# Performance work log

Measured on AMD Instinct MI355X. Metric: run time of the kernel, lower is better.

## Reference

```python
import jax, jax.numpy as jnp
import numpy as np

N_NODES = 1_000_000
N_EDGES = 16_000_000
BATCH = 1_000_000
EMBED_DIM = 3


def setup_inputs() -> dict:
    key = jax.random.key(0)
    ks = jax.random.split(key, 11)
    edge_index = jax.random.randint(ks[0], (2, N_EDGES), 0, N_NODES, dtype=jnp.int32)
    edge_weight = jax.random.uniform(ks[1], (N_EDGES,), dtype=jnp.float32) + 0.1
    home = jax.random.randint(ks[2], (BATCH,), 0, N_NODES, dtype=jnp.int32)
    away = jax.random.randint(ks[3], (BATCH,), 0, N_NODES, dtype=jnp.int32)
    emb = jax.random.normal(ks[4], (N_NODES, EMBED_DIM), dtype=jnp.float32)
    w_conv = jax.random.normal(ks[5], (3, 3), dtype=jnp.float32) * 0.5
    b_conv = jax.random.normal(ks[6], (3,), dtype=jnp.float32) * 0.1
    w1 = jax.random.normal(ks[7], (6, 6), dtype=jnp.float32) * 0.4
    b1 = jax.random.normal(ks[8], (6,), dtype=jnp.float32) * 0.1
    w3 = jax.random.normal(ks[9], (6, 3), dtype=jnp.float32) * 0.4
    b3 = jax.random.normal(ks[10], (3,), dtype=jnp.float32) * 0.1
    return {"edge_index": edge_index, "edge_weight": edge_weight, "home": home,
            "away": away, "emb": emb, "w_conv": w_conv, "b_conv": b_conv,
            "w1": w1, "b1": b1, "w3": w3, "b3": b3}


def reference(edge_index, edge_weight, home, away, emb, w_conv, b_conv, w1, b1, w3, b3):
    n = emb.shape[0]
    row, col = edge_index[0], edge_index[1]
    # gcn_norm (symmetric, add_self_loops=False): deg over target nodes
    deg = jax.ops.segment_sum(edge_weight, col, num_segments=n)
    dinv = jnp.where(deg > 0, jax.lax.rsqrt(jnp.where(deg > 0, deg, 1.0)), 0.0)
    norm = dinv[row] * edge_weight * dinv[col]  # [E]
    x = emb @ w_conv                            # [N,3] transformed features
    msg = norm[:, None] * x[row]                # [E,3] gather + scale
    agg = jax.ops.segment_sum(msg, col, num_segments=n) + b_conv  # [N,3]
    x = jax.nn.leaky_relu(agg)                  # conv1 output
    h = jnp.concatenate([x[home], x[away]], axis=-1)  # [B,6]
    h = jax.nn.leaky_relu(h @ w1 + b1)          # lin1
    h = jax.nn.leaky_relu(h @ w3 + b3)          # lin3 -> [B,3]
    return jax.nn.log_softmax(h, axis=0)        # LogSoftmax over dim=0 as in source
```

## Files before the change

### kernel.cpp

```cpp
#include <hip/hip_runtime.h>
#include <math.h>

#define NN 1000000
#define NE 16000000
#define NB 1000000
#define NEQ (NE / 4)
#define BN 4096
#define NBUCK 245
#define NBUCKR 256
#define NBLK 1024
#define SSPLIT 4
#define CMASK 0xFFFFFu

#define FPS 512.0f
#define FPINV (1.0f / 512.0f)
#define FBIAS (1 << 20)
#define FMASK 0x1FFFFFu
#define ACC_INIT 0x4000020000100000ULL

typedef int   i32x4 __attribute__((ext_vector_type(4)));
typedef float f32x4 __attribute__((ext_vector_type(4)));

__device__ __forceinline__ float leaky(float v) { return v > 0.f ? v : 0.01f * v; }

#define ATOMF(p, v) unsafeAtomicAdd((p), (v))

__device__ __forceinline__ unsigned int pack_bf32(float x, float y, float z) {
    float m = fmaxf(fmaxf(fabsf(x), fabsf(y)), fabsf(z));
    int ex = ((int)(__float_as_uint(m) >> 23) & 0xFF) - 126;
    ex = min(max(ex, -20), 11);
    float scale = __uint_as_float((unsigned int)(135 - ex) << 23);
    int qx = min(max(__float2int_rn(x * scale), -255), 255);
    int qy = min(max(__float2int_rn(y * scale), -255), 255);
    int qz = min(max(__float2int_rn(z * scale), -255), 255);
    return ((unsigned int)(qx & 0x1FF)) | ((unsigned int)(qy & 0x1FF) << 9) |
           ((unsigned int)(qz & 0x1FF) << 18) | ((unsigned int)(ex + 20) << 27);
}

__device__ __forceinline__ float3 unpack_bf32(unsigned int u) {
    int qx = ((int)(u << 23)) >> 23;
    int qy = ((int)(u << 14)) >> 23;
    int qz = ((int)(u << 5)) >> 23;
    int ex = (int)(u >> 27) - 20;
    float s = __uint_as_float((unsigned int)(ex + 119) << 23);
    return make_float3(qx * s, qy * s, qz * s);
}

__device__ __forceinline__ void atomicMaxF(float* addr, float val) {
    unsigned int* ia = (unsigned int*)addr;
    unsigned int old = *ia;
    while (true) {
        float f = __uint_as_float(old);
        if (f >= val) break;
        unsigned int prev = atomicCAS(ia, old, __float_as_uint(val));
        if (prev == old) break;
        old = prev;
    }
}

__global__ void init_stats(float* stats) {
    int t = threadIdx.x;
    if (t < 3) stats[t] = -1e30f;
    else if (t < 6) stats[t] = 0.f;
}

__global__ __launch_bounds__(256) void count_kernel(const i32x4* __restrict__ col4,
                                                    unsigned int* __restrict__ HG) {
    __shared__ unsigned int h[4][NBUCKR];
    int wave = threadIdx.x >> 6;
    for (int t = threadIdx.x; t < 4 * NBUCKR; t += 256) ((unsigned int*)h)[t] = 0u;
    __syncthreads();
    int stride = gridDim.x * 256;
    for (int i = blockIdx.x * 256 + threadIdx.x; i < NEQ; i += stride) {
        i32x4 c = __builtin_nontemporal_load(col4 + i);
        atomicAdd(&h[wave][((unsigned int)c.x) >> 12], 1u);
        atomicAdd(&h[wave][((unsigned int)c.y) >> 12], 1u);
        atomicAdd(&h[wave][((unsigned int)c.z) >> 12], 1u);
        atomicAdd(&h[wave][((unsigned int)c.w) >> 12], 1u);
    }
    __syncthreads();
    HG[(size_t)threadIdx.x * NBLK + blockIdx.x] =
        h[0][threadIdx.x] + h[1][threadIdx.x] + h[2][threadIdx.x] + h[3][threadIdx.x];
}

__global__ __launch_bounds__(256) void scan_sum(const unsigned int* __restrict__ HG,
                                                unsigned int* __restrict__ part) {
    const unsigned int* p = HG + (size_t)blockIdx.x * NBLK;
    unsigned int s = 0;
    for (int i = threadIdx.x; i < NBLK; i += 256) s += p[i];
    #pragma unroll
    for (int off = 32; off > 0; off >>= 1) s += __shfl_down(s, off);
    __shared__ unsigned int sm[4];
    int wave = threadIdx.x >> 6, lane = threadIdx.x & 63;
    if (lane == 0) sm[wave] = s;
    __syncthreads();
    if (threadIdx.x == 0) part[blockIdx.x] = sm[0] + sm[1] + sm[2] + sm[3];
}

__global__ void scan_part(unsigned int* part) {
    __shared__ unsigned int tmp[256];
    int t = threadIdx.x;
    unsigned int v = part[t];
    tmp[t] = v;
    __syncthreads();
    for (int off = 1; off < 256; off <<= 1) {
        unsigned int add = (t >= off) ? tmp[t - off] : 0u;
        __syncthreads();
        tmp[t] += add;
        __syncthreads();
    }
    part[t] = tmp[t] - v;
}

__global__ __launch_bounds__(256) void scan_apply(unsigned int* __restrict__ HG,
                                                  const unsigned int* __restrict__ part) {
    __shared__ unsigned int vals[NBLK];
    __shared__ unsigned int ts[256];
    int t = threadIdx.x;
    unsigned int* p = HG + (size_t)blockIdx.x * NBLK;
    for (int i = t; i < NBLK; i += 256) vals[i] = p[i];
    __syncthreads();
    unsigned int a0 = vals[4 * t], a1 = vals[4 * t + 1], a2 = vals[4 * t + 2], a3 = vals[4 * t + 3];
    unsigned int ls = a0 + a1 + a2 + a3;
    ts[t] = ls;
    __syncthreads();
    for (int off = 1; off < 256; off <<= 1) {
        unsigned int add = (t >= off) ? ts[t - off] : 0u;
        __syncthreads();
        ts[t] += add;
        __syncthreads();
    }
    unsigned int base = part[blockIdx.x] + ts[t] - ls;
    p[4 * t] = base;
    p[4 * t + 1] = base + a0;
    p[4 * t + 2] = base + a0 + a1;
    p[4 * t + 3] = base + a0 + a1 + a2;
}

__global__ __launch_bounds__(256) void scatter_kernel(const i32x4* __restrict__ row4,
                                                      const i32x4* __restrict__ col4,
                                                      const f32x4* __restrict__ w4,
                                                      const unsigned int* __restrict__ HG,
                                                      uint2* __restrict__ rec) {
    __shared__ unsigned int pos[NBUCKR];
    pos[threadIdx.x] = HG[(size_t)threadIdx.x * NBLK + blockIdx.x];
    __syncthreads();
    int stride = gridDim.x * 256;
    for (int i = blockIdx.x * 256 + threadIdx.x; i < NEQ; i += stride) {
        i32x4 r = __builtin_nontemporal_load(row4 + i);
        i32x4 c = __builtin_nontemporal_load(col4 + i);
        f32x4 w = __builtin_nontemporal_load(w4 + i);
        {
            unsigned int cu = (unsigned int)c.x;
            unsigned int p = atomicAdd(&pos[cu >> 12], 1u);
            rec[p] = make_uint2((unsigned int)r.x | ((cu & 4095u) << 20), __float_as_uint(w.x));
        }
        {
            unsigned int cu = (unsigned int)c.y;
            unsigned int p = atomicAdd(&pos[cu >> 12], 1u);
            rec[p] = make_uint2((unsigned int)r.y | ((cu & 4095u) << 20), __float_as_uint(w.y));
        }
        {
            unsigned int cu = (unsigned int)c.z;
            unsigned int p = atomicAdd(&pos[cu >> 12], 1u);
            rec[p] = make_uint2((unsigned int)r.z | ((cu & 4095u) << 20), __float_as_uint(w.z));
        }
        {
            unsigned int cu = (unsigned int)c.w;
            unsigned int p = atomicAdd(&pos[cu >> 12], 1u);
            rec[p] = make_uint2((unsigned int)r.w | ((cu & 4095u) << 20), __float_as_uint(w.w));
        }
    }
}

__global__ __launch_bounds__(512) void bucket_deg_kernel(const unsigned long long* __restrict__ rec,
                                                         const unsigned int* __restrict__ HG,
                                                         float* __restrict__ deg_g) {
    __shared__ float degl[BN];
    int b = blockIdx.x % NBUCK;
    int sp = blockIdx.x / NBUCK;
    for (int t = threadIdx.x; t < BN; t += 512) degl[t] = 0.f;
    unsigned int s0 = HG[(size_t)b * NBLK];
    unsigned int e0 = HG[(size_t)(b + 1) * NBLK];
    unsigned int n = e0 - s0;
    unsigned int beg = s0 + (unsigned int)((unsigned long long)n * sp / SSPLIT);
    unsigned int end = s0 + (unsigned int)((unsigned long long)n * (sp + 1) / SSPLIT);
    __syncthreads();
    unsigned int i = beg + threadIdx.x;
    for (; i + 3584 < end; i += 4096) {
        unsigned long long r[8];
        #pragma unroll
        for (int k = 0; k < 8; k++) r[k] = __builtin_nontemporal_load(rec + i + k * 512);
        #pragma unroll
        for (int k = 0; k < 8; k++)
            ATOMF(&degl[((unsigned int)r[k]) >> 20], __uint_as_float((unsigned int)(r[k] >> 32)));
    }
    for (; i < end; i += 512) {
        unsigned long long r0 = __builtin_nontemporal_load(rec + i);
        ATOMF(&degl[((unsigned int)r0) >> 20], __uint_as_float((unsigned int)(r0 >> 32)));
    }
    __syncthreads();
    int node0 = b * BN;
    for (int t = threadIdx.x; t < BN; t += 512) {
        float v = degl[t];
        if (v != 0.f) ATOMF(&deg_g[node0 + t], v);
    }
}

__global__ __launch_bounds__(256) void node1_kernel(const float* __restrict__ deg_g,
                                                    const float* __restrict__ emb,
                                                    const float* __restrict__ w_conv,
                                                    float* __restrict__ dinv,
                                                    unsigned int* __restrict__ y) {
    int g = blockIdx.x * 256 + threadIdx.x;
    if (g >= NN) return;
    float d = deg_g[g];
    float di = d > 0.f ? rsqrtf(d) : 0.f;
    dinv[g] = di;
    float e0 = emb[3 * g], e1 = emb[3 * g + 1], e2 = emb[3 * g + 2];
    float x0 = e0 * w_conv[0] + e1 * w_conv[3] + e2 * w_conv[6];
    float x1 = e0 * w_conv[1] + e1 * w_conv[4] + e2 * w_conv[7];
    float x2 = e0 * w_conv[2] + e1 * w_conv[5] + e2 * w_conv[8];
    y[g] = pack_bf32(di * x0, di * x1, di * x2);
}

__global__ __launch_bounds__(512) void bucket_agg_kernel(const unsigned long long* __restrict__ rec,
                                                         const unsigned int* __restrict__ HG,
                                                         const unsigned int* __restrict__ y,
                                                         float* __restrict__ acc_g) {
    __shared__ unsigned long long accp[BN];
    int b = blockIdx.x % NBUCK;
    int sp = blockIdx.x / NBUCK;
    for (int t = threadIdx.x; t < BN; t += 512) accp[t] = ACC_INIT;
    unsigned int s0 = HG[(size_t)b * NBLK];
    unsigned int e0 = HG[(size_t)(b + 1) * NBLK];
    unsigned int n = e0 - s0;
    unsigned int beg = s0 + (unsigned int)((unsigned long long)n * sp / SSPLIT);
    unsigned int end = s0 + (unsigned int)((unsigned long long)n * (sp + 1) / SSPLIT);
    __syncthreads();
    unsigned int i = beg + threadIdx.x;
    for (; i + 3584 < end; i += 4096) {
        unsigned long long r[8];
        #pragma unroll
        for (int k = 0; k < 8; k++) r[k] = __builtin_nontemporal_load(rec + i + k * 512);
        unsigned int yu[8];
        #pragma unroll
        for (int k = 0; k < 8; k++) yu[k] = y[((unsigned int)r[k]) & CMASK];
        #pragma unroll
        for (int k = 0; k < 8; k++) {
            float ws = __uint_as_float((unsigned int)(r[k] >> 32)) * FPS;
            float3 yv = unpack_bf32(yu[k]);
            long long q0 = (long long)__float2int_rn(ws * yv.x);
            long long q1 = (long long)__float2int_rn(ws * yv.y);
            long long q2 = (long long)__float2int_rn(ws * yv.z);
            unsigned long long term = (unsigned long long)((q2 << 42) + (q1 << 21) + q0);
            unsigned int c = ((unsigned int)r[k]) >> 20;
            atomicAdd(&accp[c], term);
        }
    }
    for (; i < end; i += 512) {
        unsigned long long r0 = __builtin_nontemporal_load(rec + i);
        float ws = __uint_as_float((unsigned int)(r0 >> 32)) * FPS;
        float3 yv = unpack_bf32(y[((unsigned int)r0) & CMASK]);
        long long q0 = (long long)__float2int_rn(ws * yv.x);
        long long q1 = (long long)__float2int_rn(ws * yv.y);
        long long q2 = (long long)__float2int_rn(ws * yv.z);
        unsigned long long term = (unsigned long long)((q2 << 42) + (q1 << 21) + q0);
        unsigned int c = ((unsigned int)r0) >> 20;
        atomicAdd(&accp[c], term);
    }
    __syncthreads();
    size_t base = (size_t)b * BN * 3;
    for (int t = threadIdx.x; t < BN; t += 512) {
        unsigned long long v = accp[t];
        if (v != ACC_INIT) {
            int f0 = (int)((unsigned int)(v & FMASK)) - FBIAS;
            int f1 = (int)((unsigned int)((v >> 21) & FMASK)) - FBIAS;
            int f2 = (int)((unsigned int)((v >> 42) & FMASK)) - FBIAS;
            if (f0) ATOMF(&acc_g[base + 3 * t + 0], (float)f0 * FPINV);
            if (f1) ATOMF(&acc_g[base + 3 * t + 1], (float)f1 * FPINV);
            if (f2) ATOMF(&acc_g[base + 3 * t + 2], (float)f2 * FPINV);
        }
    }
}

__global__ __launch_bounds__(256) void node2_kernel(const float* __restrict__ acc_g,
                                                    const float* __restrict__ dinv,
                                                    const float* __restrict__ b_conv,
                                                    unsigned int* __restrict__ xf) {
    int g = blockIdx.x * 256 + threadIdx.x;
    if (g >= NN) return;
    float di = dinv[g];
    float a0 = acc_g[3 * (size_t)g], a1 = acc_g[3 * (size_t)g + 1], a2 = acc_g[3 * (size_t)g + 2];
    xf[g] = pack_bf32(leaky(di * a0 + b_conv[0]),
                      leaky(di * a1 + b_conv[1]),
                      leaky(di * a2 + b_conv[2]));
}

__global__ __launch_bounds__(256) void batch_kernel(const i32x4* __restrict__ home4,
                                                    const i32x4* __restrict__ away4,
                                                    const unsigned int* __restrict__ xf,
                                                    const float* __restrict__ w1,
                                                    const float* __restrict__ b1,
                                                    const float* __restrict__ w3,
                                                    const float* __restrict__ b3,
                                                    float4* __restrict__ out4,
                                                    float* __restrict__ stats, int nq) {
    int i = blockIdx.x * blockDim.x + threadIdx.x;
    float m0 = -1e30f, m1 = -1e30f, m2 = -1e30f;
    if (i < nq) {
        float W1[36], B1[6], W3[18], B3[3];
        #pragma unroll
        for (int k = 0; k < 36; k++) W1[k] = w1[k];
        #pragma unroll
        for (int k = 0; k < 6; k++) B1[k] = b1[k];
        #pragma unroll
        for (int k = 0; k < 18; k++) W3[k] = w3[k];
        #pragma unroll
        for (int k = 0; k < 3; k++) B3[k] = b3[k];

        i32x4 hh = __builtin_nontemporal_load(home4 + i);
        i32x4 aa = __builtin_nontemporal_load(away4 + i);
        int hs[4] = {hh.x, hh.y, hh.z, hh.w};
        int as_[4] = {aa.x, aa.y, aa.z, aa.w};
        float o[12];
        #pragma unroll
        for (int e = 0; e < 4; e++) {
            float3 xh = unpack_bf32(xf[hs[e]]);
            float3 xa = unpack_bf32(xf[as_[e]]);
            float h[6] = {xh.x, xh.y, xh.z, xa.x, xa.y, xa.z};
            float l1v[6];
            #pragma unroll
            for (int j = 0; j < 6; j++) {
                float s = B1[j];
                #pragma unroll
                for (int k = 0; k < 6; k++) s += h[k] * W1[k * 6 + j];
                l1v[j] = leaky(s);
            }
            float o3[3];
            #pragma unroll
            for (int j = 0; j < 3; j++) {
                float s = B3[j];
                #pragma unroll
                for (int k = 0; k < 6; k++) s += l1v[k] * W3[k * 3 + j];
                o3[j] = leaky(s);
            }
            o[3 * e + 0] = o3[0];
            o[3 * e + 1] = o3[1];
            o[3 * e + 2] = o3[2];
            m0 = fmaxf(m0, o3[0]);
            m1 = fmaxf(m1, o3[1]);
            m2 = fmaxf(m2, o3[2]);
        }
        #pragma unroll
        for (int q = 0; q < 3; q++)
            out4[3 * (size_t)i + q] = make_float4(o[4 * q], o[4 * q + 1], o[4 * q + 2], o[4 * q + 3]);
    }
    #pragma unroll
    for (int off = 32; off > 0; off >>= 1) {
        m0 = fmaxf(m0, __shfl_down(m0, off));
        m1 = fmaxf(m1, __shfl_down(m1, off));
        m2 = fmaxf(m2, __shfl_down(m2, off));
    }
    __shared__ float sm[3][4];
    int wave = threadIdx.x >> 6, lane = threadIdx.x & 63;
    if (lane == 0) { sm[0][wave] = m0; sm[1][wave] = m1; sm[2][wave] = m2; }
    __syncthreads();
    if (threadIdx.x == 0) {
        atomicMaxF(&stats[0], fmaxf(fmaxf(sm[0][0], sm[0][1]), fmaxf(sm[0][2], sm[0][3])));
        atomicMaxF(&stats[1], fmaxf(fmaxf(sm[1][0], sm[1][1]), fmaxf(sm[1][2], sm[1][3])));
        atomicMaxF(&stats[2], fmaxf(fmaxf(sm[2][0], sm[2][1]), fmaxf(sm[2][2], sm[2][3])));
    }
}

__global__ __launch_bounds__(256) void sumexp_kernel(const float4* __restrict__ out4,
                                                     float* __restrict__ stats, int nq) {
    float mx0 = stats[0], mx1 = stats[1], mx2 = stats[2];
    int i = blockIdx.x * blockDim.x + threadIdx.x;
    float s0 = 0.f, s1 = 0.f, s2 = 0.f;
    if (i < nq) {
        float4 v = out4[i];
        float vals[4] = {v.x, v.y, v.z, v.w};
        int c = (4 * i) % 3;
        #pragma unroll
        for (int e = 0; e < 4; e++) {
            float mv = (c == 0) ? mx0 : ((c == 1) ? mx1 : mx2);
            float ee = expf(vals[e] - mv);
            if (c == 0) s0 += ee; else if (c == 1) s1 += ee; else s2 += ee;
            c = (c == 2) ? 0 : (c + 1);
        }
    }
    #pragma unroll
    for (int off = 32; off > 0; off >>= 1) {
        s0 += __shfl_down(s0, off);
        s1 += __shfl_down(s1, off);
        s2 += __shfl_down(s2, off);
    }
    __shared__ float sm[3][4];
    int wave = threadIdx.x >> 6, lane = threadIdx.x & 63;
    if (lane == 0) { sm[0][wave] = s0; sm[1][wave] = s1; sm[2][wave] = s2; }
    __syncthreads();
    if (threadIdx.x == 0) {
        ATOMF(&stats[3], sm[0][0] + sm[0][1] + sm[0][2] + sm[0][3]);
        ATOMF(&stats[4], sm[1][0] + sm[1][1] + sm[1][2] + sm[1][3]);
        ATOMF(&stats[5], sm[2][0] + sm[2][1] + sm[2][2] + sm[2][3]);
    }
}

__global__ __launch_bounds__(256) void final_kernel(float4* __restrict__ out4,
                                                    const float* __restrict__ stats, int nq) {
    float o0 = stats[0] + logf(stats[3]);
    float o1 = stats[1] + logf(stats[4]);
    float o2 = stats[2] + logf(stats[5]);
    int i = blockIdx.x * blockDim.x + threadIdx.x;
    if (i >= nq) return;
    float4 v = out4[i];
    float vals[4] = {v.x, v.y, v.z, v.w};
    int c = (4 * i) % 3;
    #pragma unroll
    for (int e = 0; e < 4; e++) {
        vals[e] -= (c == 0) ? o0 : ((c == 1) ? o1 : o2);
        c = (c == 2) ? 0 : (c + 1);
    }
    out4[i] = make_float4(vals[0], vals[1], vals[2], vals[3]);
}

extern "C" void kernel_launch(void* const* d_in, const int* in_sizes, int n_in,
                              void* d_out, int out_size, void* d_ws, size_t ws_size,
                              hipStream_t stream) {
    const int*   edge_index  = (const int*)d_in[0];
    const float* edge_weight = (const float*)d_in[1];
    const int*   home        = (const int*)d_in[2];
    const int*   away        = (const int*)d_in[3];
    const float* emb         = (const float*)d_in[4];
    const float* w_conv      = (const float*)d_in[5];
    const float* b_conv      = (const float*)d_in[6];
    const float* w1          = (const float*)d_in[7];
    const float* b1          = (const float*)d_in[8];
    const float* w3          = (const float*)d_in[9];
    const float* b3          = (const float*)d_in[10];
    float* out = (float*)d_out;

    char* ws = (char*)d_ws;
    uint2*        rec   = (uint2*)(ws);
    unsigned int* HG    = (unsigned int*)(ws + 128000000);
    unsigned int* part  = (unsigned int*)(ws + 129048576);
    float*        deg_g = (float*)(ws + 129049600);
    float*        dinv  = (float*)(ws + 133063680);
    unsigned int* y     = (unsigned int*)(ws + 137063680);
    float*        acc_g = (float*)(ws + 141063680);
    unsigned int* xf    = (unsigned int*)(ws + 153105920);
    float*        stats = (float*)(ws + 157105920);

    const int* row = edge_index;
    const int* col = edge_index + NE;

    init_stats<<<1, 64, 0, stream>>>(stats);
    hipMemsetAsync(deg_g, 0, 4014080, stream);
    hipMemsetAsync(acc_g, 0, 12042240, stream);

    count_kernel<<<NBLK, 256, 0, stream>>>((const i32x4*)col, HG);
    scan_sum<<<NBUCKR, 256, 0, stream>>>(HG, part);
    scan_part<<<1, 256, 0, stream>>>(part);
    scan_apply<<<NBUCKR, 256, 0, stream>>>(HG, part);
    scatter_kernel<<<NBLK, 256, 0, stream>>>((const i32x4*)row, (const i32x4*)col,
                                             (const f32x4*)edge_weight, HG, rec);

    bucket_deg_kernel<<<NBUCK * SSPLIT, 512, 0, stream>>>((const unsigned long long*)rec, HG, deg_g);
    node1_kernel<<<(NN + 255) / 256, 256, 0, stream>>>(deg_g, emb, w_conv, dinv, y);
    bucket_agg_kernel<<<NBUCK * SSPLIT, 512, 0, stream>>>((const unsigned long long*)rec, HG, y, acc_g);
    node2_kernel<<<(NN + 255) / 256, 256, 0, stream>>>(acc_g, dinv, b_conv, xf);

    const int BQ = NB / 4;
    const int OQ = (NB * 3) / 4;
    batch_kernel<<<(BQ + 255) / 256, 256, 0, stream>>>((const i32x4*)home, (const i32x4*)away, xf,
                                                       w1, b1, w3, b3, (float4*)out, stats, BQ);
    sumexp_kernel<<<(OQ + 255) / 256, 256, 0, stream>>>((const float4*)out, stats, OQ);
    final_kernel<<<(OQ + 255) / 256, 256, 0, stream>>>((float4*)out, stats, OQ);
}
```

Before: 814.5 us.

## Use 1024-node buckets owned by one block, writing results directly without global atomics

Buckets shrink from 4096 to 1024 nodes, and each bucket is now handled by exactly one block instead of being split four ways. Because of that, the degree and aggregate results are stored straight to global memory, which removes the two memsets and the global float atomics. The packed 21-bit fixed-point accumulator is decoded with signed arithmetic in node2 instead of a biased init value. In exchange there are four times as many histogram buckets, so the HG scan and the per-block position tables grow, and load balance across blocks may be worse with no split.

```diff
diff --git a/kernel.cpp b/kernel.cpp
--- a/kernel.cpp
+++ b/kernel.cpp
@@ -5,18 +5,14 @@
 #define NE 16000000
 #define NB 1000000
 #define NEQ (NE / 4)
-#define BN 4096
-#define NBUCK 245
-#define NBUCKR 256
+#define BN 1024
+#define NBUCKA 977
+#define NBUCKR 1024
 #define NBLK 1024
-#define SSPLIT 4
-#define CMASK 0xFFFFFu
+#define RMASK 0xFFFFFu
 
 #define FPS 512.0f
 #define FPINV (1.0f / 512.0f)
-#define FBIAS (1 << 20)
-#define FMASK 0x1FFFFFu
-#define ACC_INIT 0x4000020000100000ULL
 
 typedef int   i32x4 __attribute__((ext_vector_type(4)));
 typedef float f32x4 __attribute__((ext_vector_type(4)));
@@ -73,14 +69,14 @@
     int stride = gridDim.x * 256;
     for (int i = blockIdx.x * 256 + threadIdx.x; i < NEQ; i += stride) {
         i32x4 c = __builtin_nontemporal_load(col4 + i);
-        atomicAdd(&h[wave][((unsigned int)c.x) >> 12], 1u);
-        atomicAdd(&h[wave][((unsigned int)c.y) >> 12], 1u);
-        atomicAdd(&h[wave][((unsigned int)c.z) >> 12], 1u);
-        atomicAdd(&h[wave][((unsigned int)c.w) >> 12], 1u);
-    }
-    __syncthreads();
-    HG[(size_t)threadIdx.x * NBLK + blockIdx.x] =
-        h[0][threadIdx.x] + h[1][threadIdx.x] + h[2][threadIdx.x] + h[3][threadIdx.x];
+        atomicAdd(&h[wave][((unsigned int)c.x) >> 10], 1u);
+        atomicAdd(&h[wave][((unsigned int)c.y) >> 10], 1u);
+        atomicAdd(&h[wave][((unsigned int)c.z) >> 10], 1u);
+        atomicAdd(&h[wave][((unsigned int)c.w) >> 10], 1u);
+    }
+    __syncthreads();
+    for (int b = threadIdx.x; b < NBUCKR; b += 256)
+        HG[(size_t)b * NBLK + blockIdx.x] = h[0][b] + h[1][b] + h[2][b] + h[3][b];
 }
 
 __global__ __launch_bounds__(256) void scan_sum(const unsigned int* __restrict__ HG,
@@ -100,8 +96,9 @@
 __global__ void scan_part(unsigned int* part) {
     __shared__ unsigned int tmp[256];
     int t = threadIdx.x;
-    unsigned int v = part[t];
-    tmp[t] = v;
+    unsigned int v0 = part[4 * t], v1 = part[4 * t + 1], v2 = part[4 * t + 2], v3 = part[4 * t + 3];
+    unsigned int ls = v0 + v1 + v2 + v3;
+    tmp[t] = ls;
     __syncthreads();
     for (int off = 1; off < 256; off <<= 1) {
         unsigned int add = (t >= off) ? tmp[t - off] : 0u;
@@ -109,7 +106,11 @@
         tmp[t] += add;
         __syncthreads();
     }
-    part[t] = tmp[t] - v;
+    unsigned int base = tmp[t] - ls;
+    part[4 * t] = base;
+    part[4 * t + 1] = base + v0;
+    part[4 * t + 2] = base + v0 + v1;
+    part[4 * t + 3] = base + v0 + v1 + v2;
 }
 
 __global__ __launch_bounds__(256) void scan_apply(unsigned int* __restrict__ HG,
@@ -141,34 +142,26 @@
                                                       const i32x4* __restrict__ col4,
                                                       const f32x4* __restrict__ w4,
                                                       const unsigned int* __restrict__ HG,
-                                                      uint2* __restrict__ rec) {
+                                                      unsigned long long* __restrict__ rec) {
     __shared__ unsigned int pos[NBUCKR];
-    pos[threadIdx.x] = HG[(size_t)threadIdx.x * NBLK + blockIdx.x];
+    for (int b = threadIdx.x; b < NBUCKR; b += 256)
+        pos[b] = HG[(size_t)b * NBLK + blockIdx.x];
     __syncthreads();
     int stride = gridDim.x * 256;
     for (int i = blockIdx.x * 256 + threadIdx.x; i < NEQ; i += stride) {
         i32x4 r = __builtin_nontemporal_load(row4 + i);
         i32x4 c = __builtin_nontemporal_load(col4 + i);
         f32x4 w = __builtin_nontemporal_load(w4 + i);
-        {
-            unsigned int cu = (unsigned int)c.x;
-            unsigned int p = atomicAdd(&pos[cu >> 12], 1u);
-            rec[p] = make_uint2((unsigned int)r.x | ((cu & 4095u) << 20), __float_as_uint(w.x));
-        }
-        {
-            unsigned int cu = (unsigned int)c.y;
-            unsigned int p = atomicAdd(&pos[cu >> 12], 1u);
-            rec[p] = make_uint2((unsigned int)r.y | ((cu & 4095u) << 20), __float_as_uint(w.y));
-        }
-        {
-            unsigned int cu = (unsigned int)c.z;
-            unsigned int p = atomicAdd(&pos[cu >> 12], 1u);
-            rec[p] = make_uint2((unsigned int)r.z | ((cu & 4095u) << 20), __float_as_uint(w.z));
-        }
-        {
-            unsigned int cu = (unsigned int)c.w;
-            unsigned int p = atomicAdd(&pos[cu >> 12], 1u);
-            rec[p] = make_uint2((unsigned int)r.w | ((cu & 4095u) << 20), __float_as_uint(w.w));
+        int rr[4] = {r.x, r.y, r.z, r.w};
+        int cc[4] = {c.x, c.y, c.z, c.w};
+        float wf[4] = {w.x, w.y, w.z, w.w};
+        #pragma unroll
+        for (int k = 0; k < 4; k++) {
+            unsigned int cu = (unsigned int)cc[k];
+            unsigned int p = atomicAdd(&pos[cu >> 10], 1u);
+            unsigned long long rk = ((unsigned long long)__float_as_uint(wf[k]) << 32) |
+                                    ((cu & 1023u) << 20) | (unsigned int)rr[k];
+            rec[p] = rk;
         }
     }
 }
@@ -177,14 +170,10 @@
                                                          const unsigned int* __restrict__ HG,
                                                          float* __restrict__ deg_g) {
     __shared__ float degl[BN];
-    int b = blockIdx.x % NBUCK;
-    int sp = blockIdx.x / NBUCK;
+    int b = blockIdx.x;
     for (int t = threadIdx.x; t < BN; t += 512) degl[t] = 0.f;
-    unsigned int s0 = HG[(size_t)b * NBLK];
-    unsigned int e0 = HG[(size_t)(b + 1) * NBLK];
-    unsigned int n = e0 - s0;
-    unsigned int beg = s0 + (unsigned int)((unsigned long long)n * sp / SSPLIT);
-    unsigned int end = s0 + (unsigned int)((unsigned long long)n * (sp + 1) / SSPLIT);
+    unsigned int beg = HG[(size_t)b * NBLK];
+    unsigned int end = HG[(size_t)(b + 1) * NBLK];
     __syncthreads();
     unsigned int i = beg + threadIdx.x;
     for (; i + 3584 < end; i += 4096) {
@@ -193,17 +182,17 @@
         for (int k = 0; k < 8; k++) r[k] = __builtin_nontemporal_load(rec + i + k * 512);
         #pragma unroll
         for (int k = 0; k < 8; k++)
-            ATOMF(&degl[((unsigned int)r[k]) >> 20], __uint_as_float((unsigned int)(r[k] >> 32)));
+            ATOMF(&degl[(((unsigned int)r[k]) >> 20) & 1023u], __uint_as_float((unsigned int)(r[k] >> 32)));
     }
     for (; i < end; i += 512) {
         unsigned long long r0 = __builtin_nontemporal_load(rec + i);
-        ATOMF(&degl[((unsigned int)r0) >> 20], __uint_as_float((unsigned int)(r0 >> 32)));
+        ATOMF(&degl[(((unsigned int)r0) >> 20) & 1023u], __uint_as_float((unsigned int)(r0 >> 32)));
     }
     __syncthreads();
     int node0 = b * BN;
     for (int t = threadIdx.x; t < BN; t += 512) {
-        float v = degl[t];
-        if (v != 0.f) ATOMF(&deg_g[node0 + t], v);
+        int g = node0 + t;
+        if (g < NN) deg_g[g] = degl[t];
     }
 }
 
@@ -227,16 +216,12 @@
 __global__ __launch_bounds__(512) void bucket_agg_kernel(const unsigned long long* __restrict__ rec,
                                                          const unsigned int* __restrict__ HG,
                                                          const unsigned int* __restrict__ y,
-                                                         float* __restrict__ acc_g) {
+                                                         unsigned long long* __restrict__ accq) {
     __shared__ unsigned long long accp[BN];
-    int b = blockIdx.x % NBUCK;
-    int sp = blockIdx.x / NBUCK;
-    for (int t = threadIdx.x; t < BN; t += 512) accp[t] = ACC_INIT;
-    unsigned int s0 = HG[(size_t)b * NBLK];
-    unsigned int e0 = HG[(size_t)(b + 1) * NBLK];
-    unsigned int n = e0 - s0;
-    unsigned int beg = s0 + (unsigned int)((unsigned long long)n * sp / SSPLIT);
-    unsigned int end = s0 + (unsigned int)((unsigned long long)n * (sp + 1) / SSPLIT);
+    int b = blockIdx.x;
+    for (int t = threadIdx.x; t < BN; t += 512) accp[t] = 0ull;
+    unsigned int beg = HG[(size_t)b * NBLK];
+    unsigned int end = HG[(size_t)(b + 1) * NBLK];
     __syncthreads();
     unsigned int i = beg + threadIdx.x;
     for (; i + 3584 < end; i += 4096) {
@@ -245,7 +230,7 @@
         for (int k = 0; k < 8; k++) r[k] = __builtin_nontemporal_load(rec + i + k * 512);
         unsigned int yu[8];
         #pragma unroll
-        for (int k = 0; k < 8; k++) yu[k] = y[((unsigned int)r[k]) & CMASK];
+        for (int k = 0; k < 8; k++) yu[k] = y[((unsigned int)r[k]) & RMASK];
         #pragma unroll
         for (int k = 0; k < 8; k++) {
             float ws = __uint_as_float((unsigned int)(r[k] >> 32)) * FPS;
@@ -254,44 +239,44 @@
             long long q1 = (long long)__float2int_rn(ws * yv.y);
             long long q2 = (long long)__float2int_rn(ws * yv.z);
             unsigned long long term = (unsigned long long)((q2 << 42) + (q1 << 21) + q0);
-            unsigned int c = ((unsigned int)r[k]) >> 20;
+            unsigned int c = (((unsigned int)r[k]) >> 20) & 1023u;
             atomicAdd(&accp[c], term);
         }
     }
     for (; i < end; i += 512) {
         unsigned long long r0 = __builtin_nontemporal_load(rec + i);
         float ws = __uint_as_float((unsigned int)(r0 >> 32)) * FPS;
-        float3 yv = unpack_bf32(y[((unsigned int)r0) & CMASK]);
+        float3 yv = unpack_bf32(y[((unsigned int)r0) & RMASK]);
         long long q0 = (long long)__float2int_rn(ws * yv.x);
         long long q1 = (long long)__float2int_rn(ws * yv.y);
         long long q2 = (long long)__float2int_rn(ws * yv.z);
         unsigned long long term = (unsigned long long)((q2 << 42) + (q1 << 21) + q0);
-        unsigned int c = ((unsigned int)r0) >> 20;
+        unsigned int c = (((unsigned int)r0) >> 20) & 1023u;
         atomicAdd(&accp[c], term);
     }
     __syncthreads();
-    size_t base = (size_t)b * BN * 3;
+    int node0 = b * BN;
     for (int t = threadIdx.x; t < BN; t += 512) {
-        unsigned long long v = accp[t];
-        if (v != ACC_INIT) {
-            int f0 = (int)((unsigned int)(v & FMASK)) - FBIAS;
-            int f1 = (int)((unsigned int)((v >> 21) & FMASK)) - FBIAS;
-            int f2 = (int)((unsigned int)((v >> 42) & FMASK)) - FBIAS;
-            if (f0) ATOMF(&acc_g[base + 3 * t + 0], (float)f0 * FPINV);
-            if (f1) ATOMF(&acc_g[base + 3 * t + 1], (float)f1 * FPINV);
-            if (f2) ATOMF(&acc_g[base + 3 * t + 2], (float)f2 * FPINV);
-        }
-    }
-}
-
-__global__ __launch_bounds__(256) void node2_kernel(const float* __restrict__ acc_g,
+        int g = node0 + t;
+        if (g < NN) accq[g] = accp[t];
+    }
+}
+
+__global__ __launch_bounds__(256) void node2_kernel(const unsigned long long* __restrict__ accq,
                                                     const float* __restrict__ dinv,
                                                     const float* __restrict__ b_conv,
                                                     unsigned int* __restrict__ xf) {
     int g = blockIdx.x * 256 + threadIdx.x;
     if (g >= NN) return;
     float di = dinv[g];
-    float a0 = acc_g[3 * (size_t)g], a1 = acc_g[3 * (size_t)g + 1], a2 = acc_g[3 * (size_t)g + 2];
+    long long T = (long long)accq[g];
+    long long c0 = (T << 43) >> 43;
+    long long T1 = (T - c0) >> 21;
+    long long c1 = (T1 << 43) >> 43;
+    long long c2 = (T1 - c1) >> 21;
+    float a0 = (float)c0 * FPINV;
+    float a1 = (float)c1 * FPINV;
+    float a2 = (float)c2 * FPINV;
     xf[g] = pack_bf32(leaky(di * a0 + b_conv[0]),
                       leaky(di * a1 + b_conv[1]),
                       leaky(di * a2 + b_conv[2]));
@@ -442,22 +427,20 @@
     float* out = (float*)d_out;
 
     char* ws = (char*)d_ws;
-    uint2*        rec   = (uint2*)(ws);
-    unsigned int* HG    = (unsigned int*)(ws + 128000000);
-    unsigned int* part  = (unsigned int*)(ws + 129048576);
-    float*        deg_g = (float*)(ws + 129049600);
-    float*        dinv  = (float*)(ws + 133063680);
-    unsigned int* y     = (unsigned int*)(ws + 137063680);
-    float*        acc_g = (float*)(ws + 141063680);
-    unsigned int* xf    = (unsigned int*)(ws + 153105920);
-    float*        stats = (float*)(ws + 157105920);
+    unsigned long long* rec   = (unsigned long long*)(ws);
+    unsigned int*       HG    = (unsigned int*)(ws + 128000000);
+    unsigned int*       part  = (unsigned int*)(ws + 132194304);
+    float*              deg_g = (float*)(ws + 132198400);
+    float*              dinv  = (float*)(ws + 136198400);
+    unsigned int*       y     = (unsigned int*)(ws + 140198400);
+    unsigned long long* accq  = (unsigned long long*)(ws + 144198400);
+    unsigned int*       xf    = (unsigned int*)(ws + 152198400);
+    float*              stats = (float*)(ws + 156198400);
 
     const int* row = edge_index;
     const int* col = edge_index + NE;
 
     init_stats<<<1, 64, 0, stream>>>(stats);
-    hipMemsetAsync(deg_g, 0, 4014080, stream);
-    hipMemsetAsync(acc_g, 0, 12042240, stream);
 
     count_kernel<<<NBLK, 256, 0, stream>>>((const i32x4*)col, HG);
     scan_sum<<<NBUCKR, 256, 0, stream>>>(HG, part);
@@ -466,10 +449,10 @@
     scatter_kernel<<<NBLK, 256, 0, stream>>>((const i32x4*)row, (const i32x4*)col,
                                              (const f32x4*)edge_weight, HG, rec);
 
-    bucket_deg_kernel<<<NBUCK * SSPLIT, 512, 0, stream>>>((const unsigned long long*)rec, HG, deg_g);
+    bucket_deg_kernel<<<NBUCKA, 512, 0, stream>>>(rec, HG, deg_g);
     node1_kernel<<<(NN + 255) / 256, 256, 0, stream>>>(deg_g, emb, w_conv, dinv, y);
-    bucket_agg_kernel<<<NBUCK * SSPLIT, 512, 0, stream>>>((const unsigned long long*)rec, HG, y, acc_g);
-    node2_kernel<<<(NN + 255) / 256, 256, 0, stream>>>(acc_g, dinv, b_conv, xf);
+    bucket_agg_kernel<<<NBUCKA, 512, 0, stream>>>(rec, HG, y, accq);
+    node2_kernel<<<(NN + 255) / 256, 256, 0, stream>>>(accq, dinv, b_conv, xf);
 
     const int BQ = NB / 4;
     const int OQ = (NB * 3) / 4;
```

New measurement: 823.4 us. Within noise of the previous version (+1.1%).
